# Performance work log

Hardware: AMD Instinct MI355X
Metric: run time of the kernel (lower is better)

The kernel has to match this reference:

```python
import jax, jax.numpy as jnp
import numpy as np

B, N, DIM, H, HD, MLP = 32, 257, 1024, 16, 64, 4096
SCALE = HD ** -0.5


def _ln(x, w, b, eps=1e-5):
    m = x.mean(-1, keepdims=True)
    v = ((x - m) ** 2).mean(-1, keepdims=True)
    return (x - m) * jax.lax.rsqrt(v + eps) * w + b


def _quick_gelu(x):
    return x * jax.nn.sigmoid(1.702 * x)


def setup_inputs() -> dict:
    key = jax.random.key(0)
    ks = jax.random.split(key, 8)
    p = lambda k, s: jax.random.normal(k, s, jnp.float32) * 0.02
    return {
        'hidden_states': jax.random.normal(ks[0], (B, N, DIM), jnp.float32),
        'ln1_w': jnp.ones((DIM,), jnp.float32), 'ln1_b': jnp.zeros((DIM,), jnp.float32),
        'Wq': p(ks[1], (DIM, DIM)), 'bq': jnp.zeros((DIM,), jnp.float32),
        'Wk': p(ks[2], (DIM, DIM)), 'bk': jnp.zeros((DIM,), jnp.float32),
        'Wv': p(ks[3], (DIM, DIM)), 'bv': jnp.zeros((DIM,), jnp.float32),
        'Wo': p(ks[4], (DIM, DIM)), 'bo': jnp.zeros((DIM,), jnp.float32),
        'ln2_w': jnp.ones((DIM,), jnp.float32), 'ln2_b': jnp.zeros((DIM,), jnp.float32),
        'fc1_w': p(ks[5], (MLP, DIM)), 'fc1_b': jnp.zeros((MLP,), jnp.float32),
        'fc2_w': p(ks[6], (DIM, MLP)), 'fc2_b': jnp.zeros((DIM,), jnp.float32),
    }


def reference(hidden_states, ln1_w, ln1_b, Wq, bq, Wk, bk, Wv, bv, Wo, bo,
              ln2_w, ln2_b, fc1_w, fc1_b, fc2_w, fc2_b):
    x = _ln(hidden_states, ln1_w, ln1_b)            # [B,N,DIM]
    def heads(y):                                    # [B,N,DIM] -> [B,H,N,HD]
        return y.reshape(B, N, H, HD).transpose(0, 2, 1, 3)
    q = heads((x @ Wq.T + bq) * SCALE)
    k = heads(x @ Wk.T + bk)
    v = heads(x @ Wv.T + bv)
    attn_weights = jax.nn.softmax(jnp.einsum('bhnd,bhmd->bhnm', q, k), axis=-1)  # [B,H,N,N]
    ctx = jnp.einsum('bhnm,bhmd->bhnd', attn_weights, v)
    pre_proj = ctx.transpose(0, 2, 1, 3).reshape(B, N, DIM)
    attn_output = pre_proj @ Wo.T + bo
    h = hidden_states + attn_output
    residual = h
    h = _ln(h, ln2_w, ln2_b)
    h = _quick_gelu(h @ fc1_w.T + fc1_b) @ fc2_w.T + fc2_b
    hidden_out = residual + h
    # reuse_start='before_mlp': returns (pre_proj, cache_states=None, hidden, attn_weights, qkvs=None, reuse_map=None)
    return pre_proj, hidden_out, attn_weights
```

## Files before the change

kernel.cpp:

```cpp
#include <hip/hip_runtime.h>

typedef unsigned short u16;
typedef __bf16 bf16x8 __attribute__((ext_vector_type(8)));
typedef float f32x4 __attribute__((ext_vector_type(4)));
typedef unsigned short u16x8 __attribute__((ext_vector_type(8)));
typedef unsigned short u16x4 __attribute__((ext_vector_type(4)));

#define NBATCH 32
#define NTOK   257
#define DMODEL 1024
#define NHEAD  16
#define HDIM   64
#define DMLP   4096
#define MTOK   (NBATCH*NTOK)
#define MPAD   8320

__device__ __forceinline__ u16 f2bf(float f){
    unsigned int u = __float_as_uint(f);
    u = u + 0x7fffu + ((u >> 16) & 1u);
    return (u16)(u >> 16);
}

__device__ __forceinline__ f32x4 mfma16(bf16x8 a, bf16x8 b, f32x4 c){
    return __builtin_amdgcn_mfma_f32_16x16x32_bf16(a, b, c, 0, 0, 0);
}

__device__ __forceinline__ void gload16(const void* g, void* l){
    __builtin_amdgcn_global_load_lds(
        (const __attribute__((address_space(1))) unsigned int*)g,
        (__attribute__((address_space(3))) unsigned int*)l, 16, 0, 0);
}

__device__ __forceinline__ float waveSum64(float v){
    #pragma unroll
    for (int d = 1; d < 64; d <<= 1) v += __shfl_xor(v, d);
    return v;
}

__device__ __forceinline__ void xcd_swz(int &bx, int &by){
    int gx = gridDim.x;
    int nwg = gx * gridDim.y;
    int bid = blockIdx.y * gx + blockIdx.x;
    int wg = (bid & 7) * (nwg >> 3) + (bid >> 3);
    bx = wg % gx; by = wg / gx;
}

__global__ __launch_bounds__(256) void cvt_all(
        const float* __restrict__ wq, const float* __restrict__ wk,
        const float* __restrict__ wv, const float* __restrict__ wo,
        const float* __restrict__ f1, const float* __restrict__ f2,
        u16* __restrict__ dst){
    int b = blockIdx.x;
    const float* s; int rb; float sc = 1.0f;
    if (b < 1024)      { s = wq; rb = 0;    sc = 0.125f; }
    else if (b < 2048) { s = wk; rb = 1024; }
    else if (b < 3072) { s = wv; rb = 2048; }
    else if (b < 4096) { s = wo; rb = 3072; }
    else if (b < 8192) { s = f1; rb = 4096; }
    else               { s = f2; rb = 8192; }
    size_t li = ((size_t)(b - rb)*256 + threadIdx.x)*4;
    float4 v = *(const float4*)(s + li);
    u16x4 o = { f2bf(v.x*sc), f2bf(v.y*sc), f2bf(v.z*sc), f2bf(v.w*sc) };
    *(u16x4*)(dst + (size_t)b*1024 + threadIdx.x*4) = o;
}

__global__ __launch_bounds__(256) void build_bqkv(
        const float* __restrict__ bq, const float* __restrict__ bk,
        const float* __restrict__ bv, float* __restrict__ o){
    int i = blockIdx.x*256 + threadIdx.x;
    float v = (i < 1024) ? bq[i]*0.125f : ((i < 2048) ? bk[i-1024] : bv[i-2048]);
    o[i] = v;
}

__global__ __launch_bounds__(256) void ln_kernel(const float* __restrict__ x,
                                                 const float* __restrict__ w,
                                                 const float* __restrict__ b,
                                                 u16* __restrict__ y){
    int row = blockIdx.x, tid = threadIdx.x;
    float4 v = ((const float4*)(x + (size_t)row*DMODEL))[tid];
    float s = v.x + v.y + v.z + v.w;
    s = waveSum64(s);
    __shared__ float red[8];
    int wv = tid >> 6;
    if ((tid & 63) == 0) red[wv] = s;
    __syncthreads();
    float mean = (red[0]+red[1]+red[2]+red[3]) * (1.0f/1024.0f);
    float dx = v.x-mean, dy = v.y-mean, dz = v.z-mean, dw = v.w-mean;
    float s2 = dx*dx + dy*dy + dz*dz + dw*dw;
    s2 = waveSum64(s2);
    if ((tid & 63) == 0) red[4+wv] = s2;
    __syncthreads();
    float var = (red[4]+red[5]+red[6]+red[7]) * (1.0f/1024.0f);
    float rs = rsqrtf(var + 1e-5f);
    float4 wl = ((const float4*)w)[tid];
    float4 bl = ((const float4*)b)[tid];
    u16x4 o = { f2bf(dx*rs*wl.x + bl.x), f2bf(dy*rs*wl.y + bl.y),
                f2bf(dz*rs*wl.z + bl.z), f2bf(dw*rs*wl.w + bl.w) };
    ((u16x4*)(y + (size_t)row*DMODEL))[tid] = o;
}

template<int EPI>
__global__ __launch_bounds__(256) void gemm_bt(
        const u16* __restrict__ A, const u16* __restrict__ Wt,
        const float* __restrict__ bias, u16* __restrict__ outb,
        int K, int Nn, int Mvalid){
    __shared__ __align__(16) u16 As[128*64];
    __shared__ __align__(16) u16 Bs[128*64];
    int tid = threadIdx.x, lane = tid & 63, w = tid >> 6;
    int wr = w >> 1, wc = w & 1;
    int bx, by; xcd_swz(bx, by);
    int m0 = by*128, n0 = bx*128;
    int lrow = lane & 15, lk = lane >> 4;
    const f32x4 fz = {0.f,0.f,0.f,0.f};
    f32x4 acc[4][4];
    #pragma unroll
    for (int i = 0; i < 4; i++)
        #pragma unroll
        for (int j = 0; j < 4; j++) acc[i][j] = fz;

    const size_t Ks = (size_t)K;
    int so = w*1024 + lane*16;
    for (int kt = 0; kt < K; kt += 64){
        #pragma unroll
        for (int i = 0; i < 4; i++){
            int o = i*4096 + so;
            int row = o >> 7;
            int gsl = ((o >> 4) & 7) ^ (row & 7);
            gload16(A  + (size_t)(m0+row)*Ks + kt + gsl*8, &As[i*2048 + w*512]);
            gload16(Wt + (size_t)(n0+row)*Ks + kt + gsl*8, &Bs[i*2048 + w*512]);
        }
        __syncthreads();
        #pragma unroll
        for (int kk = 0; kk < 2; kk++){
            bf16x8 af[4], bfr[4];
            #pragma unroll
            for (int mi = 0; mi < 4; mi++){
                int row = wr*64 + mi*16 + lrow;
                int sl = (kk*4 + lk) ^ (row & 7);
                af[mi] = *(const bf16x8*)&As[row*64 + sl*8];
            }
            #pragma unroll
            for (int ni = 0; ni < 4; ni++){
                int row = wc*64 + ni*16 + lrow;
                int sl = (kk*4 + lk) ^ (row & 7);
                bfr[ni] = *(const bf16x8*)&Bs[row*64 + sl*8];
            }
            #pragma unroll
            for (int mi = 0; mi < 4; mi++)
                #pragma unroll
                for (int ni = 0; ni < 4; ni++)
                    acc[mi][ni] = mfma16(af[mi], bfr[ni], acc[mi][ni]);
        }
        __syncthreads();
    }
    #pragma unroll
    for (int mi = 0; mi < 4; mi++){
        #pragma unroll
        for (int ni = 0; ni < 4; ni++){
            int col = n0 + wc*64 + ni*16 + lrow;
            float bi = bias[col];
            #pragma unroll
            for (int r = 0; r < 4; r++){
                int row = m0 + wr*64 + mi*16 + lk*4 + r;
                if (row < Mvalid){
                    float v = acc[mi][ni][r] + bi;
                    size_t idx = (size_t)row*Nn + col;
                    if (EPI == 0){
                        outb[idx] = f2bf(v);
                    } else {
                        float g = v / (1.f + __expf(-1.702f*v));
                        outb[idx] = f2bf(g);
                    }
                }
            }
        }
    }
}

__global__ __launch_bounds__(256) void gemm_n64(
        const u16* __restrict__ A, const u16* __restrict__ Wt,
        const float* __restrict__ bias, const float* __restrict__ addsrc,
        float* __restrict__ outf,
        int K, int Nn, int Mvalid){
    __shared__ __align__(16) u16 As[128*64];
    __shared__ __align__(16) u16 Bs[64*64];
    int tid = threadIdx.x, lane = tid & 63, w = tid >> 6;
    int wr = w >> 1, wc = w & 1;
    int bx, by; xcd_swz(bx, by);
    int m0 = by*128, n0 = bx*64;
    int lrow = lane & 15, lk = lane >> 4;
    const f32x4 fz = {0.f,0.f,0.f,0.f};
    f32x4 acc[4][2];
    #pragma unroll
    for (int i = 0; i < 4; i++){ acc[i][0] = fz; acc[i][1] = fz; }

    const size_t Ks = (size_t)K;
    int so = w*1024 + lane*16;
    for (int kt = 0; kt < K; kt += 64){
        #pragma unroll
        for (int i = 0; i < 4; i++){
            int o = i*4096 + so;
            int row = o >> 7;
            int gsl = ((o >> 4) & 7) ^ (row & 7);
            gload16(A + (size_t)(m0+row)*Ks + kt + gsl*8, &As[i*2048 + w*512]);
        }
        #pragma unroll
        for (int i = 0; i < 2; i++){
            int o = i*4096 + so;
            int row = o >> 7;
            int gsl = ((o >> 4) & 7) ^ (row & 7);
            gload16(Wt + (size_t)(n0+row)*Ks + kt + gsl*8, &Bs[i*2048 + w*512]);
        }
        __syncthreads();
        #pragma unroll
        for (int kk = 0; kk < 2; kk++){
            bf16x8 af[4], bfr[2];
            #pragma unroll
            for (int mi = 0; mi < 4; mi++){
                int row = wr*64 + mi*16 + lrow;
                int sl = (kk*4 + lk) ^ (row & 7);
                af[mi] = *(const bf16x8*)&As[row*64 + sl*8];
            }
            #pragma unroll
            for (int ni = 0; ni < 2; ni++){
                int row = wc*32 + ni*16 + lrow;
                int sl = (kk*4 + lk) ^ (row & 7);
                bfr[ni] = *(const bf16x8*)&Bs[row*64 + sl*8];
            }
            #pragma unroll
            for (int mi = 0; mi < 4; mi++)
                #pragma unroll
                for (int ni = 0; ni < 2; ni++)
                    acc[mi][ni] = mfma16(af[mi], bfr[ni], acc[mi][ni]);
        }
        __syncthreads();
    }
    #pragma unroll
    for (int mi = 0; mi < 4; mi++){
        #pragma unroll
        for (int ni = 0; ni < 2; ni++){
            int col = n0 + wc*32 + ni*16 + lrow;
            float bi = bias[col];
            #pragma unroll
            for (int r = 0; r < 4; r++){
                int row = m0 + wr*64 + mi*16 + lk*4 + r;
                if (row < Mvalid){
                    float v = acc[mi][ni][r] + bi;
                    size_t idx = (size_t)row*Nn + col;
                    outf[idx] = addsrc[idx] + v;
                }
            }
        }
    }
}

__global__ __launch_bounds__(256) void attn_kernel(
        const u16* __restrict__ qkv, float* __restrict__ preproj,
        u16* __restrict__ ctxb, float* __restrict__ attnw){
    __shared__ __align__(16) u16 shm[18432 + 64*296];
    u16* Klds = shm;
    u16* Plds = shm;
    u16* Vt   = shm + 18432;
    int tid = threadIdx.x, lane = tid & 63, w = tid >> 6;
    int bh = blockIdx.x, bq = bh >> 4, hh = bh & 15;
    int q0 = blockIdx.y*64;
    int lrow = lane & 15, lk = lane >> 4;

    size_t base3 = ((size_t)bq*NTOK)*3072 + hh*HDIM;
    for (int c = tid; c < 2176; c += 256){
        int row = c >> 3, slot = c & 7;
        u16x8 kv = {0,0,0,0,0,0,0,0}, vv = {0,0,0,0,0,0,0,0};
        if (row < NTOK){
            kv = *(const u16x8*)(qkv + base3 + 1024 + (size_t)row*3072 + slot*8);
            vv = *(const u16x8*)(qkv + base3 + 2048 + (size_t)row*3072 + slot*8);
        }
        *(u16x8*)&Klds[row*64 + (slot ^ (row & 7))*8] = kv;
        int vr = (row < 256) ? (row ^ (slot << 3)) : row;
        #pragma unroll
        for (int j = 0; j < 8; j++) Vt[(slot*8 + j)*296 + vr] = vv[j];
    }
    for (int i = tid; i < 1536; i += 256){
        int d = i/24, c2 = 272 + (i - d*24);
        Vt[d*296 + c2] = 0;
    }
    int tok = bq*NTOK + q0 + w*16 + lrow;
    const u16* qp = qkv + (size_t)tok*3072 + hh*HDIM;
    bf16x8 qf0 = *(const bf16x8*)(qp + lk*8);
    bf16x8 qf1 = *(const bf16x8*)(qp + 32 + lk*8);
    __syncthreads();

    f32x4 S[17];
    __builtin_amdgcn_s_setprio(1);
    #pragma unroll
    for (int j = 0; j < 17; j++){
        int kcol = j*16 + lrow;
        f32x4 a = {0.f,0.f,0.f,0.f};
        bf16x8 b0 = *(const bf16x8*)&Klds[kcol*64 + ((0 + lk) ^ (kcol & 7))*8];
        a = mfma16(qf0, b0, a);
        bf16x8 b1 = *(const bf16x8*)&Klds[kcol*64 + ((4 + lk) ^ (kcol & 7))*8];
        S[j] = mfma16(qf1, b1, a);
    }
    __builtin_amdgcn_s_setprio(0);
    #pragma unroll
    for (int r = 0; r < 4; r++){
        float mx = -1e30f;
        #pragma unroll
        for (int j = 0; j < 17; j++){
            bool valid = (j < 16) || (lrow == 0);
            mx = fmaxf(mx, valid ? S[j][r] : -1e30f);
        }
        #pragma unroll
        for (int d = 1; d < 16; d <<= 1) mx = fmaxf(mx, __shfl_xor(mx, d));
        float sum = 0.f;
        #pragma unroll
        for (int j = 0; j < 17; j++){
            bool valid = (j < 16) || (lrow == 0);
            float p = valid ? __expf(S[j][r] - mx) : 0.f;
            S[j][r] = p; sum += p;
        }
        #pragma unroll
        for (int d = 1; d < 16; d <<= 1) sum += __shfl_xor(sum, d);
        float inv = 1.f / sum;
        #pragma unroll
        for (int j = 0; j < 17; j++) S[j][r] *= inv;
    }
    __syncthreads();

    for (int idx = tid; idx < 1024; idx += 256){
        int prow = idx >> 4, kk = idx & 15;
        int koff = 16 + kk;
        int slot = ((koff >> 3) ^ (prow >> 2)) & 3;
        Plds[8*2048 + prow*32 + slot*8 + (koff & 7)] = 0;
    }
    #pragma unroll
    for (int r = 0; r < 4; r++){
        int rw = lk*4 + r;
        int qrow = q0 + w*16 + rw;
        bool rowok = qrow < NTOK;
        size_t obase = ((size_t)bh*NTOK + qrow)*NTOK;
        int prow = w*16 + rw;
        #pragma unroll
        for (int j = 0; j < 17; j++){
            int col = j*16 + lrow;
            float p = S[j][r];
            if (rowok && col < NTOK) attnw[obase + col] = p;
            int kstep = col >> 5, koff = col & 31;
            int slot = ((koff >> 3) ^ (prow >> 2)) & 3;
            Plds[kstep*2048 + prow*32 + slot*8 + (koff & 7)] = f2bf(p);
        }
    }
    __syncthreads();

    f32x4 C4[4];
    #pragma unroll
    for (int n = 0; n < 4; n++) C4[n] = (f32x4){0.f,0.f,0.f,0.f};
    __builtin_amdgcn_s_setprio(1);
    #pragma unroll
    for (int ks = 0; ks < 9; ks++){
        int prow = w*16 + lrow;
        int slotp = (lk ^ (lrow >> 2)) & 3;
        bf16x8 pf = *(const bf16x8*)&Plds[ks*2048 + prow*32 + slotp*8];
        #pragma unroll
        for (int n = 0; n < 4; n++){
            int d = n*16 + lrow;
            int xv = (d >> 3) & 7;
            int kbase = ks*32 + lk*8;
            int kl = (ks < 8) ? (kbase ^ (xv << 3)) : kbase;
            bf16x8 vf = *(const bf16x8*)&Vt[d*296 + kl];
            C4[n] = mfma16(pf, vf, C4[n]);
        }
    }
    __builtin_amdgcn_s_setprio(0);
    #pragma unroll
    for (int n = 0; n < 4; n++){
        #pragma unroll
        for (int r = 0; r < 4; r++){
            int qrow = q0 + w*16 + lk*4 + r;
            if (qrow < NTOK){
                int tok2 = bq*NTOK + qrow;
                int d = hh*HDIM + n*16 + lrow;
                float v = C4[n][r];
                preproj[(size_t)tok2*DMODEL + d] = v;
                ctxb[(size_t)tok2*DMODEL + d] = f2bf(v);
            }
        }
    }
}

extern "C" void kernel_launch(void* const* d_in, const int* in_sizes, int n_in,
                              void* d_out, int out_size, void* d_ws, size_t ws_size,
                              hipStream_t stream){
    const float* hidden = (const float*)d_in[0];
    const float* ln1w = (const float*)d_in[1];
    const float* ln1b = (const float*)d_in[2];
    const float* Wq   = (const float*)d_in[3];
    const float* bq   = (const float*)d_in[4];
    const float* Wk   = (const float*)d_in[5];
    const float* bk   = (const float*)d_in[6];
    const float* Wv   = (const float*)d_in[7];
    const float* bv   = (const float*)d_in[8];
    const float* Wo   = (const float*)d_in[9];
    const float* bo   = (const float*)d_in[10];
    const float* ln2w = (const float*)d_in[11];
    const float* ln2b = (const float*)d_in[12];
    const float* fc1w = (const float*)d_in[13];
    const float* fc1b = (const float*)d_in[14];
    const float* fc2w = (const float*)d_in[15];
    const float* fc2b = (const float*)d_in[16];

    float* out0 = (float*)d_out;
    float* out1 = out0 + (size_t)MTOK*DMODEL;
    float* out2 = out1 + (size_t)MTOK*DMODEL;

    char* ws = (char*)d_ws;
    u16* qkvb = (u16*)ws;
    u16* fc1o = (u16*)ws;
    size_t off = (size_t)MPAD*DMLP*2;
    u16* xln  = (u16*)(ws + off);
    u16* ctxb = xln;
    off += (size_t)MPAD*DMODEL*2;
    u16* wbase = (u16*)(ws + off);
    u16* wqkv = wbase;
    u16* wob  = wbase + 3*1048576;
    u16* wf1  = wbase + 4*1048576;
    u16* wf2  = wbase + 8*1048576;
    off += (size_t)12*1048576*2;
    float* bqkv = (float*)(ws + off);

    cvt_all<<<12288, 256, 0, stream>>>(Wq, Wk, Wv, Wo, fc1w, fc2w, wbase);
    build_bqkv<<<12, 256, 0, stream>>>(bq, bk, bv, bqkv);

    ln_kernel<<<MTOK, 256, 0, stream>>>(hidden, ln1w, ln1b, xln);

    gemm_bt<0><<<dim3(24,65), 256, 0, stream>>>(xln, wqkv, bqkv, qkvb, 1024, 3072, MTOK);

    attn_kernel<<<dim3(512,5), 256, 0, stream>>>(qkvb, out0, ctxb, out2);

    gemm_n64<<<dim3(16,65), 256, 0, stream>>>(ctxb, wob, bo, hidden, out1, 1024, 1024, MTOK);

    ln_kernel<<<MTOK, 256, 0, stream>>>(out1, ln2w, ln2b, xln);

    gemm_bt<2><<<dim3(32,65), 256, 0, stream>>>(xln, wf1, fc1b, fc1o, 1024, 4096, MTOK);

    gemm_n64<<<dim3(16,65), 256, 0, stream>>>(fc1o, wf2, fc2b, out1, out1, 4096, 1024, MTOK);
}
```

Measured before the change: 470.2 us.

## Fuse prep kernels, enlarge GEMM M-tile to 256, loop attention over query tiles

Merges weight conversion, bias packing and the first layernorm into one launch, which removes two kernel launches. The QKV and FC1 GEMMs move to a 256x128 tile with 512 threads, so each B tile is reused across more rows. MPAD grows to cover the padded row count. The attention kernel now runs one block per (batch, head) and loops over all query tiles, so V is transposed into LDS once per head instead of once per query tile. K is now read straight from global memory rather than staged in LDS, which risks more uncoalesced traffic and fewer resident blocks in attention.

```diff
diff --git a/kernel.cpp b/kernel.cpp
--- a/kernel.cpp
+++ b/kernel.cpp
@@ -13,7 +13,7 @@
 #define HDIM   64
 #define DMLP   4096
 #define MTOK   (NBATCH*NTOK)
-#define MPAD   8320
+#define MPAD   8448
 
 __device__ __forceinline__ u16 f2bf(float f){
     unsigned int u = __float_as_uint(f);
@@ -45,31 +45,56 @@
     bx = wg % gx; by = wg / gx;
 }
 
-__global__ __launch_bounds__(256) void cvt_all(
+__global__ __launch_bounds__(256) void prep_all(
         const float* __restrict__ wq, const float* __restrict__ wk,
         const float* __restrict__ wv, const float* __restrict__ wo,
         const float* __restrict__ f1, const float* __restrict__ f2,
-        u16* __restrict__ dst){
-    int b = blockIdx.x;
-    const float* s; int rb; float sc = 1.0f;
-    if (b < 1024)      { s = wq; rb = 0;    sc = 0.125f; }
-    else if (b < 2048) { s = wk; rb = 1024; }
-    else if (b < 3072) { s = wv; rb = 2048; }
-    else if (b < 4096) { s = wo; rb = 3072; }
-    else if (b < 8192) { s = f1; rb = 4096; }
-    else               { s = f2; rb = 8192; }
-    size_t li = ((size_t)(b - rb)*256 + threadIdx.x)*4;
-    float4 v = *(const float4*)(s + li);
-    u16x4 o = { f2bf(v.x*sc), f2bf(v.y*sc), f2bf(v.z*sc), f2bf(v.w*sc) };
-    *(u16x4*)(dst + (size_t)b*1024 + threadIdx.x*4) = o;
-}
-
-__global__ __launch_bounds__(256) void build_bqkv(
+        u16* __restrict__ dst,
+        const float* __restrict__ hidden, const float* __restrict__ ln1w,
+        const float* __restrict__ ln1b, u16* __restrict__ xln,
         const float* __restrict__ bq, const float* __restrict__ bk,
-        const float* __restrict__ bv, float* __restrict__ o){
-    int i = blockIdx.x*256 + threadIdx.x;
-    float v = (i < 1024) ? bq[i]*0.125f : ((i < 2048) ? bk[i-1024] : bv[i-2048]);
-    o[i] = v;
+        const float* __restrict__ bv, float* __restrict__ bqkv){
+    int b = blockIdx.x, tid = threadIdx.x;
+    if (b < 12288){
+        const float* s; int rb; float sc = 1.0f;
+        if (b < 1024)      { s = wq; rb = 0;    sc = 0.125f; }
+        else if (b < 2048) { s = wk; rb = 1024; }
+        else if (b < 3072) { s = wv; rb = 2048; }
+        else if (b < 4096) { s = wo; rb = 3072; }
+        else if (b < 8192) { s = f1; rb = 4096; }
+        else               { s = f2; rb = 8192; }
+        size_t li = ((size_t)(b - rb)*256 + tid)*4;
+        float4 v = *(const float4*)(s + li);
+        u16x4 o = { f2bf(v.x*sc), f2bf(v.y*sc), f2bf(v.z*sc), f2bf(v.w*sc) };
+        *(u16x4*)(dst + (size_t)b*1024 + tid*4) = o;
+    } else if (b < 12288 + MTOK){
+        int row = b - 12288;
+        float4 v = ((const float4*)(hidden + (size_t)row*DMODEL))[tid];
+        float s = v.x + v.y + v.z + v.w;
+        s = waveSum64(s);
+        __shared__ float red[8];
+        int wv2 = tid >> 6;
+        if ((tid & 63) == 0) red[wv2] = s;
+        __syncthreads();
+        float mean = (red[0]+red[1]+red[2]+red[3]) * (1.0f/1024.0f);
+        float dx = v.x-mean, dy = v.y-mean, dz = v.z-mean, dw = v.w-mean;
+        float s2 = dx*dx + dy*dy + dz*dz + dw*dw;
+        s2 = waveSum64(s2);
+        if ((tid & 63) == 0) red[4+wv2] = s2;
+        __syncthreads();
+        float var = (red[4]+red[5]+red[6]+red[7]) * (1.0f/1024.0f);
+        float rs = rsqrtf(var + 1e-5f);
+        float4 wl = ((const float4*)ln1w)[tid];
+        float4 bl = ((const float4*)ln1b)[tid];
+        u16x4 o = { f2bf(dx*rs*wl.x + bl.x), f2bf(dy*rs*wl.y + bl.y),
+                    f2bf(dz*rs*wl.z + bl.z), f2bf(dw*rs*wl.w + bl.w) };
+        ((u16x4*)(xln + (size_t)row*DMODEL))[tid] = o;
+    } else {
+        int i = (b - 12288 - MTOK)*256 + tid;
+        float v = (i < 1024) ? bq[i]*0.125f
+                             : ((i < 2048) ? bk[i-1024] : bv[i-2048]);
+        bqkv[i] = v;
+    }
 }
 
 __global__ __launch_bounds__(256) void ln_kernel(const float* __restrict__ x,
@@ -100,16 +125,16 @@
 }
 
 template<int EPI>
-__global__ __launch_bounds__(256) void gemm_bt(
+__global__ __launch_bounds__(512) void gemm_t256(
         const u16* __restrict__ A, const u16* __restrict__ Wt,
         const float* __restrict__ bias, u16* __restrict__ outb,
         int K, int Nn, int Mvalid){
-    __shared__ __align__(16) u16 As[128*64];
+    __shared__ __align__(16) u16 As[256*64];
     __shared__ __align__(16) u16 Bs[128*64];
     int tid = threadIdx.x, lane = tid & 63, w = tid >> 6;
     int wr = w >> 1, wc = w & 1;
     int bx, by; xcd_swz(bx, by);
-    int m0 = by*128, n0 = bx*128;
+    int m0 = by*256, n0 = bx*128;
     int lrow = lane & 15, lk = lane >> 4;
     const f32x4 fz = {0.f,0.f,0.f,0.f};
     f32x4 acc[4][4];
@@ -123,11 +148,17 @@
     for (int kt = 0; kt < K; kt += 64){
         #pragma unroll
         for (int i = 0; i < 4; i++){
-            int o = i*4096 + so;
+            int o = i*8192 + so;
             int row = o >> 7;
             int gsl = ((o >> 4) & 7) ^ (row & 7);
-            gload16(A  + (size_t)(m0+row)*Ks + kt + gsl*8, &As[i*2048 + w*512]);
-            gload16(Wt + (size_t)(n0+row)*Ks + kt + gsl*8, &Bs[i*2048 + w*512]);
+            gload16(A + (size_t)(m0+row)*Ks + kt + gsl*8, &As[i*4096 + w*512]);
+        }
+        #pragma unroll
+        for (int i = 0; i < 2; i++){
+            int o = i*8192 + so;
+            int row = o >> 7;
+            int gsl = ((o >> 4) & 7) ^ (row & 7);
+            gload16(Wt + (size_t)(n0+row)*Ks + kt + gsl*8, &Bs[i*4096 + w*512]);
         }
         __syncthreads();
         #pragma unroll
@@ -165,11 +196,11 @@
                 if (row < Mvalid){
                     float v = acc[mi][ni][r] + bi;
                     size_t idx = (size_t)row*Nn + col;
-                    if (EPI == 0){
-                        outb[idx] = f2bf(v);
-                    } else {
+                    if (EPI == 2){
                         float g = v / (1.f + __expf(-1.702f*v));
                         outb[idx] = f2bf(g);
+                    } else {
+                        outb[idx] = f2bf(v);
                     }
                 }
             }
@@ -257,24 +288,19 @@
 __global__ __launch_bounds__(256) void attn_kernel(
         const u16* __restrict__ qkv, float* __restrict__ preproj,
         u16* __restrict__ ctxb, float* __restrict__ attnw){
-    __shared__ __align__(16) u16 shm[18432 + 64*296];
-    u16* Klds = shm;
-    u16* Plds = shm;
-    u16* Vt   = shm + 18432;
+    __shared__ __align__(16) u16 Vt[64*296];
+    __shared__ __align__(16) u16 Plds[9*64*32];
     int tid = threadIdx.x, lane = tid & 63, w = tid >> 6;
     int bh = blockIdx.x, bq = bh >> 4, hh = bh & 15;
-    int q0 = blockIdx.y*64;
     int lrow = lane & 15, lk = lane >> 4;
 
     size_t base3 = ((size_t)bq*NTOK)*3072 + hh*HDIM;
+    const u16* Kg = qkv + base3 + 1024;
     for (int c = tid; c < 2176; c += 256){
         int row = c >> 3, slot = c & 7;
-        u16x8 kv = {0,0,0,0,0,0,0,0}, vv = {0,0,0,0,0,0,0,0};
-        if (row < NTOK){
-            kv = *(const u16x8*)(qkv + base3 + 1024 + (size_t)row*3072 + slot*8);
+        u16x8 vv = {0,0,0,0,0,0,0,0};
+        if (row < NTOK)
             vv = *(const u16x8*)(qkv + base3 + 2048 + (size_t)row*3072 + slot*8);
-        }
-        *(u16x8*)&Klds[row*64 + (slot ^ (row & 7))*8] = kv;
         int vr = (row < 256) ? (row ^ (slot << 3)) : row;
         #pragma unroll
         for (int j = 0; j < 8; j++) Vt[(slot*8 + j)*296 + vr] = vv[j];
@@ -283,105 +309,108 @@
         int d = i/24, c2 = 272 + (i - d*24);
         Vt[d*296 + c2] = 0;
     }
-    int tok = bq*NTOK + q0 + w*16 + lrow;
-    const u16* qp = qkv + (size_t)tok*3072 + hh*HDIM;
-    bf16x8 qf0 = *(const bf16x8*)(qp + lk*8);
-    bf16x8 qf1 = *(const bf16x8*)(qp + 32 + lk*8);
-    __syncthreads();
-
-    f32x4 S[17];
-    __builtin_amdgcn_s_setprio(1);
-    #pragma unroll
-    for (int j = 0; j < 17; j++){
-        int kcol = j*16 + lrow;
-        f32x4 a = {0.f,0.f,0.f,0.f};
-        bf16x8 b0 = *(const bf16x8*)&Klds[kcol*64 + ((0 + lk) ^ (kcol & 7))*8];
-        a = mfma16(qf0, b0, a);
-        bf16x8 b1 = *(const bf16x8*)&Klds[kcol*64 + ((4 + lk) ^ (kcol & 7))*8];
-        S[j] = mfma16(qf1, b1, a);
-    }
-    __builtin_amdgcn_s_setprio(0);
-    #pragma unroll
-    for (int r = 0; r < 4; r++){
-        float mx = -1e30f;
-        #pragma unroll
-        for (int j = 0; j < 17; j++){
-            bool valid = (j < 16) || (lrow == 0);
-            mx = fmaxf(mx, valid ? S[j][r] : -1e30f);
-        }
-        #pragma unroll
-        for (int d = 1; d < 16; d <<= 1) mx = fmaxf(mx, __shfl_xor(mx, d));
-        float sum = 0.f;
-        #pragma unroll
-        for (int j = 0; j < 17; j++){
-            bool valid = (j < 16) || (lrow == 0);
-            float p = valid ? __expf(S[j][r] - mx) : 0.f;
-            S[j][r] = p; sum += p;
-        }
-        #pragma unroll
-        for (int d = 1; d < 16; d <<= 1) sum += __shfl_xor(sum, d);
-        float inv = 1.f / sum;
-        #pragma unroll
-        for (int j = 0; j < 17; j++) S[j][r] *= inv;
-    }
-    __syncthreads();
-
     for (int idx = tid; idx < 1024; idx += 256){
         int prow = idx >> 4, kk = idx & 15;
         int koff = 16 + kk;
         int slot = ((koff >> 3) ^ (prow >> 2)) & 3;
         Plds[8*2048 + prow*32 + slot*8 + (koff & 7)] = 0;
     }
-    #pragma unroll
-    for (int r = 0; r < 4; r++){
-        int rw = lk*4 + r;
-        int qrow = q0 + w*16 + rw;
-        bool rowok = qrow < NTOK;
-        size_t obase = ((size_t)bh*NTOK + qrow)*NTOK;
-        int prow = w*16 + rw;
+
+    for (int q0 = 0; q0 < 320; q0 += 64){
+        int tok = bq*NTOK + q0 + w*16 + lrow;
+        const u16* qp = qkv + (size_t)tok*3072 + hh*HDIM;
+        bf16x8 qf0 = *(const bf16x8*)(qp + lk*8);
+        bf16x8 qf1 = *(const bf16x8*)(qp + 32 + lk*8);
+
+        f32x4 S[17];
+        __builtin_amdgcn_s_setprio(1);
         #pragma unroll
         for (int j = 0; j < 17; j++){
-            int col = j*16 + lrow;
-            float p = S[j][r];
-            if (rowok && col < NTOK) attnw[obase + col] = p;
-            int kstep = col >> 5, koff = col & 31;
-            int slot = ((koff >> 3) ^ (prow >> 2)) & 3;
-            Plds[kstep*2048 + prow*32 + slot*8 + (koff & 7)] = f2bf(p);
-        }
-    }
-    __syncthreads();
-
-    f32x4 C4[4];
-    #pragma unroll
-    for (int n = 0; n < 4; n++) C4[n] = (f32x4){0.f,0.f,0.f,0.f};
-    __builtin_amdgcn_s_setprio(1);
-    #pragma unroll
-    for (int ks = 0; ks < 9; ks++){
-        int prow = w*16 + lrow;
-        int slotp = (lk ^ (lrow >> 2)) & 3;
-        bf16x8 pf = *(const bf16x8*)&Plds[ks*2048 + prow*32 + slotp*8];
+            int kcol = j*16 + lrow;
+            const u16* kp = Kg + (size_t)kcol*3072;
+            f32x4 a = {0.f,0.f,0.f,0.f};
+            bf16x8 b0 = *(const bf16x8*)(kp + lk*8);
+            a = mfma16(qf0, b0, a);
+            bf16x8 b1 = *(const bf16x8*)(kp + 32 + lk*8);
+            S[j] = mfma16(qf1, b1, a);
+        }
+        __builtin_amdgcn_s_setprio(0);
+        #pragma unroll
+        for (int r = 0; r < 4; r++){
+            float mx = -1e30f;
+            #pragma unroll
+            for (int j = 0; j < 17; j++){
+                bool valid = (j < 16) || (lrow == 0);
+                mx = fmaxf(mx, valid ? S[j][r] : -1e30f);
+            }
+            #pragma unroll
+            for (int d = 1; d < 16; d <<= 1) mx = fmaxf(mx, __shfl_xor(mx, d));
+            float sum = 0.f;
+            #pragma unroll
+            for (int j = 0; j < 17; j++){
+                bool valid = (j < 16) || (lrow == 0);
+                float p = valid ? __expf(S[j][r] - mx) : 0.f;
+                S[j][r] = p; sum += p;
+            }
+            #pragma unroll
+            for (int d = 1; d < 16; d <<= 1) sum += __shfl_xor(sum, d);
+            float inv = 1.f / sum;
+            #pragma unroll
+            for (int j = 0; j < 17; j++) S[j][r] *= inv;
+        }
+        __syncthreads();
+
+        #pragma unroll
+        for (int r = 0; r < 4; r++){
+            int rw = lk*4 + r;
+            int qrow = q0 + w*16 + rw;
+            bool rowok = qrow < NTOK;
+            size_t obase = ((size_t)bh*NTOK + qrow)*NTOK;
+            int prow = w*16 + rw;
+            #pragma unroll
+            for (int j = 0; j < 17; j++){
+                int col = j*16 + lrow;
+                float p = S[j][r];
+                if (rowok && col < NTOK) attnw[obase + col] = p;
+                int kstep = col >> 5, koff = col & 31;
+                int slot = ((koff >> 3) ^ (prow >> 2)) & 3;
+                Plds[kstep*2048 + prow*32 + slot*8 + (koff & 7)] = f2bf(p);
+            }
+        }
+        __syncthreads();
+
+        f32x4 C4[4];
+        #pragma unroll
+        for (int n = 0; n < 4; n++) C4[n] = (f32x4){0.f,0.f,0.f,0.f};
+        __builtin_amdgcn_s_setprio(1);
+        #pragma unroll
+        for (int ks = 0; ks < 9; ks++){
+            int prow = w*16 + lrow;
+            int slotp = (lk ^ (lrow >> 2)) & 3;
+            bf16x8 pf = *(const bf16x8*)&Plds[ks*2048 + prow*32 + slotp*8];
+            #pragma unroll
+            for (int n = 0; n < 4; n++){
+                int d = n*16 + lrow;
+                int xv = (d >> 3) & 7;
+                int kbase = ks*32 + lk*8;
+                int kl = (ks < 8) ? (kbase ^ (xv << 3)) : kbase;
+                bf16x8 vf = *(const bf16x8*)&Vt[d*296 + kl];
+                C4[n] = mfma16(pf, vf, C4[n]);
+            }
+        }
+        __builtin_amdgcn_s_setprio(0);
         #pragma unroll
         for (int n = 0; n < 4; n++){
-            int d = n*16 + lrow;
-            int xv = (d >> 3) & 7;
-            int kbase = ks*32 + lk*8;
-            int kl = (ks < 8) ? (kbase ^ (xv << 3)) : kbase;
-            bf16x8 vf = *(const bf16x8*)&Vt[d*296 + kl];
-            C4[n] = mfma16(pf, vf, C4[n]);
-        }
-    }
-    __builtin_amdgcn_s_setprio(0);
-    #pragma unroll
-    for (int n = 0; n < 4; n++){
-        #pragma unroll
-        for (int r = 0; r < 4; r++){
-            int qrow = q0 + w*16 + lk*4 + r;
-            if (qrow < NTOK){
-                int tok2 = bq*NTOK + qrow;
-                int d = hh*HDIM + n*16 + lrow;
-                float v = C4[n][r];
-                preproj[(size_t)tok2*DMODEL + d] = v;
-                ctxb[(size_t)tok2*DMODEL + d] = f2bf(v);
+            #pragma unroll
+            for (int r = 0; r < 4; r++){
+                int qrow = q0 + w*16 + lk*4 + r;
+                if (qrow < NTOK){
+                    int tok2 = bq*NTOK + qrow;
+                    int d = hh*HDIM + n*16 + lrow;
+                    float v = C4[n][r];
+                    preproj[(size_t)tok2*DMODEL + d] = v;
+                    ctxb[(size_t)tok2*DMODEL + d] = f2bf(v);
+                }
             }
         }
     }
@@ -427,20 +456,20 @@
     off += (size_t)12*1048576*2;
     float* bqkv = (float*)(ws + off);
 
-    cvt_all<<<12288, 256, 0, stream>>>(Wq, Wk, Wv, Wo, fc1w, fc2w, wbase);
-    build_bqkv<<<12, 256, 0, stream>>>(bq, bk, bv, bqkv);
-
-    ln_kernel<<<MTOK, 256, 0, stream>>>(hidden, ln1w, ln1b, xln);
-
-    gemm_bt<0><<<dim3(24,65), 256, 0, stream>>>(xln, wqkv, bqkv, qkvb, 1024, 3072, MTOK);
-
-    attn_kernel<<<dim3(512,5), 256, 0, stream>>>(qkvb, out0, ctxb, out2);
+    prep_all<<<12288 + MTOK + 12, 256, 0, stream>>>(
+        Wq, Wk, Wv, Wo, fc1w, fc2w, wbase,
+        hidden, ln1w, ln1b, xln,
+        bq, bk, bv, bqkv);
+
+    gemm_t256<0><<<dim3(24,33), 512, 0, stream>>>(xln, wqkv, bqkv, qkvb, 1024, 3072, MTOK);
+
+    attn_kernel<<<dim3(512,1), 256, 0, stream>>>(qkvb, out0, ctxb, out2);
 
     gemm_n64<<<dim3(16,65), 256, 0, stream>>>(ctxb, wob, bo, hidden, out1, 1024, 1024, MTOK);
 
     ln_kernel<<<MTOK, 256, 0, stream>>>(out1, ln2w, ln2b, xln);
 
-    gemm_bt<2><<<dim3(32,65), 256, 0, stream>>>(xln, wf1, fc1b, fc1o, 1024, 4096, MTOK);
+    gemm_t256<2><<<dim3(32,33), 512, 0, stream>>>(xln, wf1, fc1b, fc1o, 1024, 4096, MTOK);
 
     gemm_n64<<<dim3(16,65), 256, 0, stream>>>(fc1o, wf2, fc2b, out1, out1, 4096, 1024, MTOK);
 }
```

Result: faster. 440.3 us (-6.4%).
